# Performance work log

Measured on AMD Instinct MI355X. Metric: run time of the kernel, lower is better.

Reference implementation:

```python
import jax, jax.numpy as jnp
import numpy as np

H = 512  # hidden_size


def setup_inputs() -> dict:
    key = jax.random.key(0)
    k1, k2, k3, k4, k5 = jax.random.split(key, 5)
    B, S = 32, 2048
    hidden = jax.random.normal(k1, (1, B, H), dtype=jnp.float32)
    encoder_outputs = jax.random.normal(k2, (B, S, 2 * H), dtype=jnp.float32)
    # nn.Linear(3H, H): weight [H, 3H], store transposed [3H, H] for x @ W
    scale_a = 1.0 / np.sqrt(3 * H)
    Wa = jax.random.uniform(k3, (3 * H, H), jnp.float32, -scale_a, scale_a)
    ba = jax.random.uniform(k4, (H,), jnp.float32, -scale_a, scale_a)
    # nn.Linear(H, 1, bias=False): weight [1, H] -> store as [H]
    scale_v = 1.0 / np.sqrt(H)
    v = jax.random.uniform(k5, (H,), jnp.float32, -scale_v, scale_v)
    return {"hidden": hidden, "encoder_outputs": encoder_outputs,
            "Wa": Wa, "ba": ba, "v": v}


def reference(hidden, encoder_outputs, Wa, ba, v):
    # hidden: [1, B, H] -> [B, H]; encoder_outputs: [B, S, 2H]
    h = jnp.squeeze(hidden, axis=0)                      # [B, H]
    # Split concat-linear into two projections (same math as cat + matmul):
    Wh, We = Wa[:H], Wa[H:]                              # [H, H], [2H, H]
    # energy: [B, S, H] = tanh(h Wh + enc We + b), h broadcast over S
    energy = jnp.tanh(h @ Wh + jnp.einsum('bse,eh->bsh', encoder_outputs, We)[..., :, :] + ba) if False else \
             jnp.tanh((h @ Wh)[:, None, :] + jnp.einsum('bse,eh->bsh', encoder_outputs, We) + ba)
    scores = jnp.einsum('bsh,h->bs', energy, v)          # [B, S]
    attention_weights = jax.nn.softmax(scores, axis=1)   # [B, S]
    context = jnp.einsum('bs,bse->be', attention_weights, encoder_outputs)  # [B, 2H]
    return context, attention_weights
```

## Files before the change

### kernel.cpp

```cpp
#include <hip/hip_runtime.h>

typedef unsigned short ushort_t;
typedef __attribute__((ext_vector_type(8))) short bf16x8;
typedef __attribute__((ext_vector_type(4))) float f32x4;

#define H 512
#define E 1024
#define S 2048
#define B 32

__device__ __forceinline__ ushort_t f2bf(float f) {
    unsigned u = __float_as_uint(f);
    unsigned r = (u + 0x7FFFu + ((u >> 16) & 1u)) >> 16;
    return (ushort_t)r;
}

__global__ void prep_hb(const float* __restrict__ hidden, const float* __restrict__ Wa,
                        const float* __restrict__ ba, float* __restrict__ hb) {
    int b = blockIdx.x, tid = threadIdx.x;
    __shared__ float hs[H];
    hs[tid]       = hidden[b * H + tid];
    hs[tid + 256] = hidden[b * H + tid + 256];
    __syncthreads();
    float a0 = 0.f, a1 = 0.f;
    for (int k = 0; k < H; ++k) {
        float hv = hs[k];
        a0 += hv * Wa[(size_t)k * H + tid];
        a1 += hv * Wa[(size_t)k * H + tid + 256];
    }
    hb[b * H + tid]       = a0 + ba[tid];
    hb[b * H + tid + 256] = a1 + ba[tid + 256];
}

__global__ void prep_wef(const float* __restrict__ Wa, ushort_t* __restrict__ wef) {
    int g = blockIdx.x * 256 + threadIdx.x;
    int kt = g >> 11, nt = (g >> 6) & 31, l = g & 63;
    int kbase = kt * 32 + ((l >> 4) << 3);
    int n = nt * 16 + (l & 15);
    #pragma unroll
    for (int j = 0; j < 8; ++j)
        wef[(size_t)g * 8 + j] = f2bf(Wa[(size_t)(H + kbase + j) * H + n]);
}

__launch_bounds__(256, 2)
__global__ void score_kernel(const float* __restrict__ enc, const ushort_t* __restrict__ wef,
                             const float* __restrict__ hb, const float* __restrict__ v,
                             float* __restrict__ scores) {
    int b = blockIdx.y;
    int s0 = blockIdx.x * 64;
    int tid = threadIdx.x;
    int wave = tid >> 6, lane = tid & 63;
    int q = lane >> 4, nl = lane & 15;

    __shared__ ushort_t As[64 * 72];
    __shared__ float sred[4][64];

    f32x4 acc[4][8] = {};

    const float* Arow = enc + ((size_t)b * S + s0) * E;
    int srow = tid >> 3;
    int scol = (tid & 7) * 8;

    for (int kb = 0; kb < 16; ++kb) {
        #pragma unroll
        for (int it = 0; it < 2; ++it) {
            int r = srow + it * 32;
            const float* src = Arow + (size_t)r * E + kb * 64 + scol;
            float4 x = *(const float4*)src;
            float4 y = *(const float4*)(src + 4);
            uint4 u;
            u.x = (unsigned)f2bf(x.x) | ((unsigned)f2bf(x.y) << 16);
            u.y = (unsigned)f2bf(x.z) | ((unsigned)f2bf(x.w) << 16);
            u.z = (unsigned)f2bf(y.x) | ((unsigned)f2bf(y.y) << 16);
            u.w = (unsigned)f2bf(y.z) | ((unsigned)f2bf(y.w) << 16);
            *(uint4*)&As[r * 72 + scol] = u;
        }
        __syncthreads();
        #pragma unroll
        for (int ks = 0; ks < 2; ++ks) {
            int kt = kb * 2 + ks;
            bf16x8 afr[4];
            #pragma unroll
            for (int mt = 0; mt < 4; ++mt) {
                int m = mt * 16 + nl;
                afr[mt] = *(const bf16x8*)&As[m * 72 + ks * 32 + q * 8];
            }
            #pragma unroll
            for (int ntl = 0; ntl < 8; ++ntl) {
                int nt = wave * 8 + ntl;
                bf16x8 bfr = *(const bf16x8*)&wef[((size_t)(kt * 32 + nt) * 64 + lane) * 8];
                #pragma unroll
                for (int mt = 0; mt < 4; ++mt)
                    acc[mt][ntl] = __builtin_amdgcn_mfma_f32_16x16x32_bf16(
                        afr[mt], bfr, acc[mt][ntl], 0, 0, 0);
            }
        }
        __syncthreads();
    }

    float p[16];
    #pragma unroll
    for (int i = 0; i < 16; ++i) p[i] = 0.f;
    #pragma unroll
    for (int ntl = 0; ntl < 8; ++ntl) {
        int n = wave * 128 + ntl * 16 + nl;
        float hv = hb[b * H + n];
        float vv = v[n];
        #pragma unroll
        for (int mt = 0; mt < 4; ++mt)
            #pragma unroll
            for (int r = 0; r < 4; ++r)
                p[mt * 4 + r] += vv * tanhf(acc[mt][ntl][r] + hv);
    }
    #pragma unroll
    for (int off = 1; off < 16; off <<= 1) {
        #pragma unroll
        for (int i = 0; i < 16; ++i) p[i] += __shfl_xor(p[i], off, 64);
    }
    if (nl == 0) {
        #pragma unroll
        for (int mt = 0; mt < 4; ++mt)
            #pragma unroll
            for (int r = 0; r < 4; ++r)
                sred[wave][mt * 16 + q * 4 + r] = p[mt * 4 + r];
    }
    __syncthreads();
    if (tid < 64) {
        float s = sred[0][tid] + sred[1][tid] + sred[2][tid] + sred[3][tid];
        scores[(size_t)b * S + s0 + tid] = s;
    }
}

__global__ void softmax_kernel(const float* __restrict__ scores, float* __restrict__ out) {
    int b = blockIdx.x, tid = threadIdx.x;
    const float* row = scores + (size_t)b * S;
    float loc[8];
    float mx = -3.4e38f;
    #pragma unroll
    for (int i = 0; i < 8; ++i) { loc[i] = row[tid + i * 256]; mx = fmaxf(mx, loc[i]); }
    #pragma unroll
    for (int off = 32; off > 0; off >>= 1) mx = fmaxf(mx, __shfl_xor(mx, off, 64));
    __shared__ float wm[4], wsm[4];
    if ((tid & 63) == 0) wm[tid >> 6] = mx;
    __syncthreads();
    mx = fmaxf(fmaxf(wm[0], wm[1]), fmaxf(wm[2], wm[3]));
    float sum = 0.f;
    #pragma unroll
    for (int i = 0; i < 8; ++i) { loc[i] = __expf(loc[i] - mx); sum += loc[i]; }
    #pragma unroll
    for (int off = 32; off > 0; off >>= 1) sum += __shfl_xor(sum, off, 64);
    if ((tid & 63) == 0) wsm[tid >> 6] = sum;
    __syncthreads();
    sum = wsm[0] + wsm[1] + wsm[2] + wsm[3];
    float inv = 1.f / sum;
    #pragma unroll
    for (int i = 0; i < 8; ++i) out[B * E + (size_t)b * S + tid + i * 256] = loc[i] * inv;
    #pragma unroll
    for (int i = 0; i < 4; ++i) out[(size_t)b * E + tid + i * 256] = 0.f;
}

__global__ void context_kernel(const float* __restrict__ enc, const float* __restrict__ w_attn,
                               float* __restrict__ out_ctx) {
    int et = blockIdx.x, sc = blockIdx.y, b = blockIdx.z;
    int e = et * 256 + threadIdx.x;
    const float* w  = w_attn + (size_t)b * S + sc * 256;
    const float* ep = enc + ((size_t)b * S + sc * 256) * E + e;
    float acc = 0.f;
    #pragma unroll 4
    for (int s = 0; s < 256; ++s) acc += w[s] * ep[(size_t)s * E];
    atomicAdd(&out_ctx[(size_t)b * E + e], acc);
}

extern "C" void kernel_launch(void* const* d_in, const int* in_sizes, int n_in,
                              void* d_out, int out_size, void* d_ws, size_t ws_size,
                              hipStream_t stream) {
    const float* hidden = (const float*)d_in[0];
    const float* enc    = (const float*)d_in[1];
    const float* Wa     = (const float*)d_in[2];
    const float* ba     = (const float*)d_in[3];
    const float* v      = (const float*)d_in[4];
    float* out = (float*)d_out;

    char* ws = (char*)d_ws;
    ushort_t* wef = (ushort_t*)ws;
    float* hb     = (float*)(ws + (1 << 20));
    float* scores = (float*)(ws + (1 << 20) + (1 << 16));

    prep_hb<<<B, 256, 0, stream>>>(hidden, Wa, ba, hb);
    prep_wef<<<256, 256, 0, stream>>>(Wa, wef);
    score_kernel<<<dim3(S / 64, B), 256, 0, stream>>>(enc, wef, hb, v, scores);
    softmax_kernel<<<B, 256, 0, stream>>>(scores, out);
    context_kernel<<<dim3(4, 8, B), 256, 0, stream>>>(enc, out + B * E, out);
}
```

Before: 539.4 us.

## Double-buffer score tile with register prefetch, split-K prep_hb, widen context loads

The score kernel now prefetches the next fp32 encoder tile into registers while the current tile is converted to bf16 and stored into one of two LDS buffers. This replaces the two __syncthreads per step with a single lgkmcnt wait plus barrier, so global load latency can overlap MFMA work. prep_hb is split over 8 K-chunks per batch row, with atomic accumulation into a zero-initialised buffer, to raise its parallelism. The context kernel uses float2 loads and a finer S split. The changes cost extra LDS and registers, which may lower occupancy, and add atomics plus a memset launch.

```diff
diff --git a/kernel.cpp b/kernel.cpp
--- a/kernel.cpp
+++ b/kernel.cpp
@@ -17,19 +17,18 @@
 
 __global__ void prep_hb(const float* __restrict__ hidden, const float* __restrict__ Wa,
                         const float* __restrict__ ba, float* __restrict__ hb) {
-    int b = blockIdx.x, tid = threadIdx.x;
-    __shared__ float hs[H];
-    hs[tid]       = hidden[b * H + tid];
-    hs[tid + 256] = hidden[b * H + tid + 256];
-    __syncthreads();
+    int b = blockIdx.x, kc = blockIdx.y, tid = threadIdx.x;
+    const float* hp = hidden + b * H + kc * 64;
     float a0 = 0.f, a1 = 0.f;
-    for (int k = 0; k < H; ++k) {
-        float hv = hs[k];
-        a0 += hv * Wa[(size_t)k * H + tid];
-        a1 += hv * Wa[(size_t)k * H + tid + 256];
-    }
-    hb[b * H + tid]       = a0 + ba[tid];
-    hb[b * H + tid + 256] = a1 + ba[tid + 256];
+    #pragma unroll 8
+    for (int k = 0; k < 64; ++k) {
+        float hv = hp[k];
+        a0 += hv * Wa[(size_t)(kc * 64 + k) * H + tid];
+        a1 += hv * Wa[(size_t)(kc * 64 + k) * H + tid + 256];
+    }
+    if (kc == 0) { a0 += ba[tid]; a1 += ba[tid + 256]; }
+    atomicAdd(&hb[b * H + tid], a0);
+    atomicAdd(&hb[b * H + tid + 256], a1);
 }
 
 __global__ void prep_wef(const float* __restrict__ Wa, ushort_t* __restrict__ wef) {
@@ -52,7 +51,7 @@
     int wave = tid >> 6, lane = tid & 63;
     int q = lane >> 4, nl = lane & 15;
 
-    __shared__ ushort_t As[64 * 72];
+    __shared__ ushort_t As[2][64 * 72];
     __shared__ float sred[4][64];
 
     f32x4 acc[4][8] = {};
@@ -61,21 +60,38 @@
     int srow = tid >> 3;
     int scol = (tid & 7) * 8;
 
+    const float* src0 = Arow + (size_t)srow * E + scol;
+    const float* src1 = Arow + (size_t)(srow + 32) * E + scol;
+
+    float4 x0 = *(const float4*)(src0);
+    float4 y0 = *(const float4*)(src0 + 4);
+    float4 x1 = *(const float4*)(src1);
+    float4 y1 = *(const float4*)(src1 + 4);
+
     for (int kb = 0; kb < 16; ++kb) {
-        #pragma unroll
-        for (int it = 0; it < 2; ++it) {
-            int r = srow + it * 32;
-            const float* src = Arow + (size_t)r * E + kb * 64 + scol;
-            float4 x = *(const float4*)src;
-            float4 y = *(const float4*)(src + 4);
-            uint4 u;
-            u.x = (unsigned)f2bf(x.x) | ((unsigned)f2bf(x.y) << 16);
-            u.y = (unsigned)f2bf(x.z) | ((unsigned)f2bf(x.w) << 16);
-            u.z = (unsigned)f2bf(y.x) | ((unsigned)f2bf(y.y) << 16);
-            u.w = (unsigned)f2bf(y.z) | ((unsigned)f2bf(y.w) << 16);
-            *(uint4*)&As[r * 72 + scol] = u;
+        ushort_t* Ab = &As[kb & 1][0];
+        uint4 u0, u1;
+        u0.x = (unsigned)f2bf(x0.x) | ((unsigned)f2bf(x0.y) << 16);
+        u0.y = (unsigned)f2bf(x0.z) | ((unsigned)f2bf(x0.w) << 16);
+        u0.z = (unsigned)f2bf(y0.x) | ((unsigned)f2bf(y0.y) << 16);
+        u0.w = (unsigned)f2bf(y0.z) | ((unsigned)f2bf(y0.w) << 16);
+        u1.x = (unsigned)f2bf(x1.x) | ((unsigned)f2bf(x1.y) << 16);
+        u1.y = (unsigned)f2bf(x1.z) | ((unsigned)f2bf(x1.w) << 16);
+        u1.z = (unsigned)f2bf(y1.x) | ((unsigned)f2bf(y1.y) << 16);
+        u1.w = (unsigned)f2bf(y1.z) | ((unsigned)f2bf(y1.w) << 16);
+        *(uint4*)&Ab[srow * 72 + scol]        = u0;
+        *(uint4*)&Ab[(srow + 32) * 72 + scol] = u1;
+
+        if (kb < 15) {
+            int off = (kb + 1) * 64;
+            x0 = *(const float4*)(src0 + off);
+            y0 = *(const float4*)(src0 + off + 4);
+            x1 = *(const float4*)(src1 + off);
+            y1 = *(const float4*)(src1 + off + 4);
         }
-        __syncthreads();
+
+        __asm__ __volatile__("s_waitcnt lgkmcnt(0)\n\ts_barrier" ::: "memory");
+
         #pragma unroll
         for (int ks = 0; ks < 2; ++ks) {
             int kt = kb * 2 + ks;
@@ -83,7 +99,7 @@
             #pragma unroll
             for (int mt = 0; mt < 4; ++mt) {
                 int m = mt * 16 + nl;
-                afr[mt] = *(const bf16x8*)&As[m * 72 + ks * 32 + q * 8];
+                afr[mt] = *(const bf16x8*)&Ab[m * 72 + ks * 32 + q * 8];
             }
             #pragma unroll
             for (int ntl = 0; ntl < 8; ++ntl) {
@@ -95,7 +111,6 @@
                         afr[mt], bfr, acc[mt][ntl], 0, 0, 0);
             }
         }
-        __syncthreads();
     }
 
     float p[16];
@@ -162,13 +177,19 @@
 __global__ void context_kernel(const float* __restrict__ enc, const float* __restrict__ w_attn,
                                float* __restrict__ out_ctx) {
     int et = blockIdx.x, sc = blockIdx.y, b = blockIdx.z;
-    int e = et * 256 + threadIdx.x;
-    const float* w  = w_attn + (size_t)b * S + sc * 256;
-    const float* ep = enc + ((size_t)b * S + sc * 256) * E + e;
-    float acc = 0.f;
-    #pragma unroll 4
-    for (int s = 0; s < 256; ++s) acc += w[s] * ep[(size_t)s * E];
-    atomicAdd(&out_ctx[(size_t)b * E + e], acc);
+    int e = et * 512 + threadIdx.x * 2;
+    const float* w  = w_attn + (size_t)b * S + sc * 128;
+    const float* ep = enc + ((size_t)b * S + sc * 128) * E + e;
+    float a0 = 0.f, a1 = 0.f;
+    #pragma unroll 8
+    for (int s = 0; s < 128; ++s) {
+        float ws = w[s];
+        float2 x = *(const float2*)(ep + (size_t)s * E);
+        a0 += ws * x.x;
+        a1 += ws * x.y;
+    }
+    atomicAdd(&out_ctx[(size_t)b * E + e], a0);
+    atomicAdd(&out_ctx[(size_t)b * E + e + 1], a1);
 }
 
 extern "C" void kernel_launch(void* const* d_in, const int* in_sizes, int n_in,
@@ -186,9 +207,10 @@
     float* hb     = (float*)(ws + (1 << 20));
     float* scores = (float*)(ws + (1 << 20) + (1 << 16));
 
-    prep_hb<<<B, 256, 0, stream>>>(hidden, Wa, ba, hb);
+    hipMemsetAsync(hb, 0, B * H * sizeof(float), stream);
+    prep_hb<<<dim3(B, 8), 256, 0, stream>>>(hidden, Wa, ba, hb);
     prep_wef<<<256, 256, 0, stream>>>(Wa, wef);
     score_kernel<<<dim3(S / 64, B), 256, 0, stream>>>(enc, wef, hb, v, scores);
     softmax_kernel<<<B, 256, 0, stream>>>(scores, out);
-    context_kernel<<<dim3(4, 8, B), 256, 0, stream>>>(enc, out + B * E, out);
-}
+    context_kernel<<<dim3(2, 16, B), 256, 0, stream>>>(enc, out + B * E, out);
+}
```

Result: faster. 516.2 us (-4.3%).
